# Optimization experiments

Hardware: AMD Instinct MI355X
Metric: run time of the kernel (lower is better)

## Reference

```python
import jax, jax.numpy as jnp
import numpy as np

NUM_HEADS = 8
N_NODES = 50000
N_EDGES = 800000
# irreps_value = 128x0e + 64x1o -> fused block sizes [128, 192]; per-head sizes [16, 24]
FUSED_BLOCKS = [128, 192]
HEAD_SIZES = [16, 24]
VALUE_DIM = sum(FUSED_BLOCKS)  # 320


def unfuse_value(x):
    # [E, 320] -> [E, H, 40], splitting per irrep block then reshaping to heads
    parts, start = [], 0
    for blk, hsz in zip(FUSED_BLOCKS, HEAD_SIZES):
        parts.append(x[:, start:start + blk].reshape(x.shape[0], NUM_HEADS, hsz))
        start += blk
    return jnp.concatenate(parts, axis=2)


def fuse_value(x):
    # [N, H, 40] -> [N, 320]
    parts, start = [], 0
    for hsz in HEAD_SIZES:
        parts.append(x[:, :, start:start + hsz].reshape(x.shape[0], NUM_HEADS * hsz))
        start += hsz
    return jnp.concatenate(parts, axis=1)


def edge_softmax(w, dst, num_nodes):
    # segmented (per destination node) softmax over edges, per head
    m = jax.ops.segment_max(w, dst, num_segments=num_nodes)
    m = jnp.where(jnp.isfinite(m), m, 0.0)  # nodes with no incoming edges
    e = jnp.exp(w - m[dst])
    s = jax.ops.segment_sum(e, dst, num_segments=num_nodes)
    return e / s[dst]


def setup_inputs() -> dict:
    key = jax.random.key(0)
    k1, k2, k3, k4 = jax.random.split(key, 4)
    value = jax.random.normal(k1, (N_EDGES, VALUE_DIM), dtype=jnp.float32)
    edge_weights = jax.random.normal(k2, (N_EDGES, NUM_HEADS), dtype=jnp.float32)
    edge_weights_cutoff = jax.random.uniform(k3, (N_EDGES,), dtype=jnp.float32)
    edge_index = jax.random.randint(k4, (2, N_EDGES), 0, N_NODES, dtype=jnp.int64)
    return {"value": value, "edge_weights": edge_weights,
            "edge_weights_cutoff": edge_weights_cutoff, "edge_index": edge_index}


def reference(value, edge_weights, edge_weights_cutoff, edge_index):
    dst = edge_index[1]
    v = unfuse_value(value)                              # [E, H, 40]
    w = edge_weights_cutoff[:, None] * edge_weights      # [E, H]
    a = edge_softmax(w, dst, N_NODES)                    # [E, H]
    f = jax.ops.segment_sum(a[:, :, None] * v, dst, num_segments=N_NODES)  # [N, H, 40]
    return fuse_value(f)                                 # [N, 320]
```

## Files before the change

kernel.cpp:

```cpp
#include <hip/hip_runtime.h>
#include <hip/hip_bf16.h>
#include <stdint.h>

#define N_NODES 50000
#define N_EDGES 800000
#define NH 8
#define VD 320

typedef float f32x4 __attribute__((ext_vector_type(4)));

__global__ void k_init(unsigned* __restrict__ cnt, unsigned* __restrict__ total) {
    int i = blockIdx.x * blockDim.x + threadIdx.x;
    int stride = gridDim.x * blockDim.x;
    for (int j = i; j < N_NODES; j += stride) cnt[j] = 0u;
    if (i == 0) *total = 0u;
}

__global__ __launch_bounds__(256) void k_exp(
        const float* __restrict__ ew, const float* __restrict__ cutoff,
        const int* __restrict__ dst, unsigned* __restrict__ cnt,
        float* __restrict__ expw) {
    int e = blockIdx.x * 256 + threadIdx.x;
    if (e >= N_EDGES) return;
    float cw = cutoff[e];
    const f32x4* ewv = reinterpret_cast<const f32x4*>(ew + (size_t)e * NH);
    f32x4 w0 = ewv[0], w1 = ewv[1];
    f32x4 p0, p1;
    p0.x = __expf(cw * w0.x); p0.y = __expf(cw * w0.y);
    p0.z = __expf(cw * w0.z); p0.w = __expf(cw * w0.w);
    p1.x = __expf(cw * w1.x); p1.y = __expf(cw * w1.y);
    p1.z = __expf(cw * w1.z); p1.w = __expf(cw * w1.w);
    f32x4* ov = reinterpret_cast<f32x4*>(expw + (size_t)e * NH);
    ov[0] = p0; ov[1] = p1;
    atomicAdd(&cnt[dst[e]], 1u);
}

__global__ __launch_bounds__(256) void k_ranges(
        const unsigned* __restrict__ cnt, unsigned* __restrict__ rowstart,
        unsigned* __restrict__ cursor, unsigned* __restrict__ total) {
    int i = blockIdx.x * 256 + threadIdx.x;
    int lane = threadIdx.x & 63;
    unsigned c = (i < N_NODES) ? cnt[i] : 0u;
    unsigned incl = c;
    #pragma unroll
    for (int off = 1; off < 64; off <<= 1) {
        unsigned v = __shfl_up(incl, off, 64);
        if (lane >= off) incl += v;
    }
    unsigned wave_total = __shfl(incl, 63, 64);
    unsigned base = 0;
    if (lane == 63) base = atomicAdd(total, wave_total);
    base = __shfl(base, 63, 64);
    if (i < N_NODES) {
        unsigned st = base + incl - c;
        rowstart[i] = st;
        cursor[i] = st;
    }
}

__global__ __launch_bounds__(256) void k_scatter(
        const int* __restrict__ dst, unsigned* __restrict__ cursor,
        unsigned* __restrict__ eid) {
    int e = blockIdx.x * 256 + threadIdx.x;
    if (e >= N_EDGES) return;
    unsigned pos = atomicAdd(&cursor[dst[e]], 1u);
    eid[pos] = (unsigned)e;
}

__global__ __launch_bounds__(320) void k_gather(
        const float* __restrict__ expw, const float* __restrict__ value,
        const unsigned* __restrict__ rowstart, const unsigned* __restrict__ cnt,
        const unsigned* __restrict__ eid, float* __restrict__ out) {
    int t = threadIdx.x;
    int cg = t % 80;
    int ns = t / 80;
    int c = cg * 4;
    int h = (c < 128) ? (c >> 4) : ((c - 128) / 24);
    for (int n = blockIdx.x * 4 + ns; n < N_NODES; n += gridDim.x * 4) {
        unsigned k0 = rowstart[n];
        unsigned deg = cnt[n];
        float sx = 0.f, sy = 0.f, sz = 0.f, sw = 0.f, se = 0.f;
        unsigned k = 0;
        for (; k + 4 <= deg; k += 4) {
            unsigned e0 = eid[k0 + k],     e1 = eid[k0 + k + 1];
            unsigned e2 = eid[k0 + k + 2], e3 = eid[k0 + k + 3];
            float a0 = expw[e0 * NH + h], a1 = expw[e1 * NH + h];
            float a2 = expw[e2 * NH + h], a3 = expw[e3 * NH + h];
            f32x4 v0 = __builtin_nontemporal_load(
                reinterpret_cast<const f32x4*>(value + (size_t)(e0 * VD + c)));
            f32x4 v1 = __builtin_nontemporal_load(
                reinterpret_cast<const f32x4*>(value + (size_t)(e1 * VD + c)));
            f32x4 v2 = __builtin_nontemporal_load(
                reinterpret_cast<const f32x4*>(value + (size_t)(e2 * VD + c)));
            f32x4 v3 = __builtin_nontemporal_load(
                reinterpret_cast<const f32x4*>(value + (size_t)(e3 * VD + c)));
            se += (a0 + a1) + (a2 + a3);
            sx += a0 * v0.x + a1 * v1.x + a2 * v2.x + a3 * v3.x;
            sy += a0 * v0.y + a1 * v1.y + a2 * v2.y + a3 * v3.y;
            sz += a0 * v0.z + a1 * v1.z + a2 * v2.z + a3 * v3.z;
            sw += a0 * v0.w + a1 * v1.w + a2 * v2.w + a3 * v3.w;
        }
        for (; k < deg; ++k) {
            unsigned e = eid[k0 + k];
            float a = expw[e * NH + h];
            f32x4 v = __builtin_nontemporal_load(
                reinterpret_cast<const f32x4*>(value + (size_t)(e * VD + c)));
            se += a;
            sx += a * v.x; sy += a * v.y; sz += a * v.z; sw += a * v.w;
        }
        float scale = (deg > 0) ? 1.0f / se : 0.0f;
        f32x4 r;
        r.x = sx * scale; r.y = sy * scale; r.z = sz * scale; r.w = sw * scale;
        __builtin_nontemporal_store(r,
            reinterpret_cast<f32x4*>(out + (size_t)n * VD + c));
    }
}

extern "C" void kernel_launch(void* const* d_in, const int* in_sizes, int n_in,
                              void* d_out, int out_size, void* d_ws, size_t ws_size,
                              hipStream_t stream) {
    const float* value  = (const float*)d_in[0];
    const float* ew     = (const float*)d_in[1];
    const float* cutoff = (const float*)d_in[2];
    const int*   eidx   = (const int*)d_in[3];
    const int*   dst    = eidx + N_EDGES;
    float* out = (float*)d_out;

    char* ws = (char*)d_ws;
    float*    expw     = (float*)ws;    ws += (size_t)N_EDGES * NH * 4;
    unsigned* cnt      = (unsigned*)ws; ws += (size_t)((N_NODES + 3) & ~3) * 4;
    unsigned* rowstart = (unsigned*)ws; ws += (size_t)((N_NODES + 3) & ~3) * 4;
    unsigned* cursor   = (unsigned*)ws; ws += (size_t)((N_NODES + 3) & ~3) * 4;
    unsigned* eid      = (unsigned*)ws; ws += (size_t)N_EDGES * 4;
    unsigned* total    = (unsigned*)ws; ws += 16;

    const int gE = (N_EDGES + 255) / 256;
    const int gN = (N_NODES + 255) / 256;

    k_init<<<196, 256, 0, stream>>>(cnt, total);
    k_exp<<<gE, 256, 0, stream>>>(ew, cutoff, dst, cnt, expw);
    k_ranges<<<gN, 256, 0, stream>>>(cnt, rowstart, cursor, total);
    k_scatter<<<gE, 256, 0, stream>>>(dst, cursor, eid);
    k_gather<<<2048, 320, 0, stream>>>(expw, value, rowstart, cnt, eid, out);
}
```

Before: 345.4 us.

## Fuse exp into gather, pack cutoff with edge ids, wave-per-node with shuffles

Removes the separate exp pass and its 25.6MB expw buffer. The cutoff is stored alongside each edge id in the CSR array, and exp(cutoff*w) is computed inside the gather. The gather now maps one 64-lane wave to each node: the wave loads up to 64 CSR entries at once and broadcasts them with shuffles, and lanes 0-15 also handle the remaining 64 columns. The cost is recomputing the exp per column group and an unbalanced second pass that only 16 lanes execute.

```diff
diff --git a/kernel.cpp b/kernel.cpp
--- a/kernel.cpp
+++ b/kernel.cpp
@@ -16,22 +16,10 @@
     if (i == 0) *total = 0u;
 }
 
-__global__ __launch_bounds__(256) void k_exp(
-        const float* __restrict__ ew, const float* __restrict__ cutoff,
-        const int* __restrict__ dst, unsigned* __restrict__ cnt,
-        float* __restrict__ expw) {
+__global__ __launch_bounds__(256) void k_hist(
+        const int* __restrict__ dst, unsigned* __restrict__ cnt) {
     int e = blockIdx.x * 256 + threadIdx.x;
     if (e >= N_EDGES) return;
-    float cw = cutoff[e];
-    const f32x4* ewv = reinterpret_cast<const f32x4*>(ew + (size_t)e * NH);
-    f32x4 w0 = ewv[0], w1 = ewv[1];
-    f32x4 p0, p1;
-    p0.x = __expf(cw * w0.x); p0.y = __expf(cw * w0.y);
-    p0.z = __expf(cw * w0.z); p0.w = __expf(cw * w0.w);
-    p1.x = __expf(cw * w1.x); p1.y = __expf(cw * w1.y);
-    p1.z = __expf(cw * w1.z); p1.w = __expf(cw * w1.w);
-    f32x4* ov = reinterpret_cast<f32x4*>(expw + (size_t)e * NH);
-    ov[0] = p0; ov[1] = p1;
     atomicAdd(&cnt[dst[e]], 1u);
 }
 
@@ -59,60 +47,74 @@
 }
 
 __global__ __launch_bounds__(256) void k_scatter(
-        const int* __restrict__ dst, unsigned* __restrict__ cursor,
-        unsigned* __restrict__ eid) {
+        const int* __restrict__ dst, const float* __restrict__ cutoff,
+        unsigned* __restrict__ cursor, uint2* __restrict__ csr) {
     int e = blockIdx.x * 256 + threadIdx.x;
     if (e >= N_EDGES) return;
     unsigned pos = atomicAdd(&cursor[dst[e]], 1u);
-    eid[pos] = (unsigned)e;
+    uint2 p; p.x = (unsigned)e; p.y = __float_as_uint(cutoff[e]);
+    csr[pos] = p;
 }
 
-__global__ __launch_bounds__(320) void k_gather(
-        const float* __restrict__ expw, const float* __restrict__ value,
+__global__ __launch_bounds__(256) void k_gather(
+        const float* __restrict__ ew, const float* __restrict__ value,
         const unsigned* __restrict__ rowstart, const unsigned* __restrict__ cnt,
-        const unsigned* __restrict__ eid, float* __restrict__ out) {
-    int t = threadIdx.x;
-    int cg = t % 80;
-    int ns = t / 80;
-    int c = cg * 4;
+        const uint2* __restrict__ csr, float* __restrict__ out) {
+    int lane = threadIdx.x & 63;
+    int wslot = blockIdx.x * 4 + (threadIdx.x >> 6);
+    int nslots = gridDim.x * 4;
+    int c = lane * 4;
     int h = (c < 128) ? (c >> 4) : ((c - 128) / 24);
-    for (int n = blockIdx.x * 4 + ns; n < N_NODES; n += gridDim.x * 4) {
+    int c2 = 256 + c;
+    int h2 = (c2 - 128) / 24;
+    bool sec = lane < 16;
+    for (int n = wslot; n < N_NODES; n += nslots) {
         unsigned k0 = rowstart[n];
         unsigned deg = cnt[n];
-        float sx = 0.f, sy = 0.f, sz = 0.f, sw = 0.f, se = 0.f;
-        unsigned k = 0;
-        for (; k + 4 <= deg; k += 4) {
-            unsigned e0 = eid[k0 + k],     e1 = eid[k0 + k + 1];
-            unsigned e2 = eid[k0 + k + 2], e3 = eid[k0 + k + 3];
-            float a0 = expw[e0 * NH + h], a1 = expw[e1 * NH + h];
-            float a2 = expw[e2 * NH + h], a3 = expw[e3 * NH + h];
-            f32x4 v0 = __builtin_nontemporal_load(
-                reinterpret_cast<const f32x4*>(value + (size_t)(e0 * VD + c)));
-            f32x4 v1 = __builtin_nontemporal_load(
-                reinterpret_cast<const f32x4*>(value + (size_t)(e1 * VD + c)));
-            f32x4 v2 = __builtin_nontemporal_load(
-                reinterpret_cast<const f32x4*>(value + (size_t)(e2 * VD + c)));
-            f32x4 v3 = __builtin_nontemporal_load(
-                reinterpret_cast<const f32x4*>(value + (size_t)(e3 * VD + c)));
-            se += (a0 + a1) + (a2 + a3);
-            sx += a0 * v0.x + a1 * v1.x + a2 * v2.x + a3 * v3.x;
-            sy += a0 * v0.y + a1 * v1.y + a2 * v2.y + a3 * v3.y;
-            sz += a0 * v0.z + a1 * v1.z + a2 * v2.z + a3 * v3.z;
-            sw += a0 * v0.w + a1 * v1.w + a2 * v2.w + a3 * v3.w;
+        f32x4 acc = {0.f, 0.f, 0.f, 0.f}, acc2 = {0.f, 0.f, 0.f, 0.f};
+        float se = 0.f, se2 = 0.f;
+        for (unsigned base = 0; base < deg; base += 64) {
+            unsigned m = deg - base; if (m > 64u) m = 64u;
+            unsigned pe = 0u, pc = 0u;
+            if (lane < (int)m) {
+                uint2 p = csr[k0 + base + lane];
+                pe = p.x; pc = p.y;
+            }
+            #pragma unroll 2
+            for (unsigned j = 0; j < m; ++j) {
+                unsigned e = (unsigned)__shfl((int)pe, (int)j, 64);
+                float cu = __uint_as_float(__shfl((int)pc, (int)j, 64));
+                const float* vrow = value + (size_t)e * VD;
+                float w = ew[(size_t)e * NH + h];
+                f32x4 v = __builtin_nontemporal_load(
+                    reinterpret_cast<const f32x4*>(vrow + c));
+                float a = __expf(cu * w);
+                se += a;
+                acc.x += a * v.x; acc.y += a * v.y;
+                acc.z += a * v.z; acc.w += a * v.w;
+                if (sec) {
+                    float w2 = ew[(size_t)e * NH + h2];
+                    f32x4 v2 = __builtin_nontemporal_load(
+                        reinterpret_cast<const f32x4*>(vrow + c2));
+                    float a2 = __expf(cu * w2);
+                    se2 += a2;
+                    acc2.x += a2 * v2.x; acc2.y += a2 * v2.y;
+                    acc2.z += a2 * v2.z; acc2.w += a2 * v2.w;
+                }
+            }
         }
-        for (; k < deg; ++k) {
-            unsigned e = eid[k0 + k];
-            float a = expw[e * NH + h];
-            f32x4 v = __builtin_nontemporal_load(
-                reinterpret_cast<const f32x4*>(value + (size_t)(e * VD + c)));
-            se += a;
-            sx += a * v.x; sy += a * v.y; sz += a * v.z; sw += a * v.w;
-        }
-        float scale = (deg > 0) ? 1.0f / se : 0.0f;
-        f32x4 r;
-        r.x = sx * scale; r.y = sy * scale; r.z = sz * scale; r.w = sw * scale;
+        float sc = (deg > 0) ? 1.0f / se : 0.0f;
+        f32x4 r; r.x = acc.x * sc; r.y = acc.y * sc;
+        r.z = acc.z * sc; r.w = acc.w * sc;
         __builtin_nontemporal_store(r,
             reinterpret_cast<f32x4*>(out + (size_t)n * VD + c));
+        if (sec) {
+            float sc2 = (deg > 0) ? 1.0f / se2 : 0.0f;
+            f32x4 r2; r2.x = acc2.x * sc2; r2.y = acc2.y * sc2;
+            r2.z = acc2.z * sc2; r2.w = acc2.w * sc2;
+            __builtin_nontemporal_store(r2,
+                reinterpret_cast<f32x4*>(out + (size_t)n * VD + c2));
+        }
     }
 }
 
@@ -127,19 +129,18 @@
     float* out = (float*)d_out;
 
     char* ws = (char*)d_ws;
-    float*    expw     = (float*)ws;    ws += (size_t)N_EDGES * NH * 4;
     unsigned* cnt      = (unsigned*)ws; ws += (size_t)((N_NODES + 3) & ~3) * 4;
     unsigned* rowstart = (unsigned*)ws; ws += (size_t)((N_NODES + 3) & ~3) * 4;
     unsigned* cursor   = (unsigned*)ws; ws += (size_t)((N_NODES + 3) & ~3) * 4;
-    unsigned* eid      = (unsigned*)ws; ws += (size_t)N_EDGES * 4;
     unsigned* total    = (unsigned*)ws; ws += 16;
+    uint2*    csr      = (uint2*)ws;    ws += (size_t)N_EDGES * 8;
 
     const int gE = (N_EDGES + 255) / 256;
     const int gN = (N_NODES + 255) / 256;
 
     k_init<<<196, 256, 0, stream>>>(cnt, total);
-    k_exp<<<gE, 256, 0, stream>>>(ew, cutoff, dst, cnt, expw);
+    k_hist<<<gE, 256, 0, stream>>>(dst, cnt);
     k_ranges<<<gN, 256, 0, stream>>>(cnt, rowstart, cursor, total);
-    k_scatter<<<gE, 256, 0, stream>>>(dst, cursor, eid);
-    k_gather<<<2048, 320, 0, stream>>>(expw, value, rowstart, cnt, eid, out);
+    k_scatter<<<gE, 256, 0, stream>>>(dst, cutoff, cursor, csr);
+    k_gather<<<2048, 256, 0, stream>>>(ew, value, rowstart, cnt, csr, out);
 }
```

Result: no change. 340.1 us (-1.5%).
